# Kernel optimization log

Hardware: AMD Instinct MI355X
Metric: run time of the kernel (lower is better)

Reference implementation:

```python
import jax, jax.numpy as jnp
import numpy as np

HEADS = 4
DIM_HEAD = 32
DIM = 128
B, N, Hq, Wg = 2, 6, 32, 32   # batch, cameras, BEV grid
HK, WK = 28, 60               # image feature map


def _ln(x, g, b, eps=1e-5):
    mu = jnp.mean(x, axis=-1, keepdims=True)
    var = jnp.mean((x - mu) ** 2, axis=-1, keepdims=True)
    return (x - mu) * jax.lax.rsqrt(var + eps) * g + b


def setup_inputs() -> dict:
    key = jax.random.key(0)
    ks = jax.random.split(key, 12)
    s = 0.05  # weight scale to keep softmax logits well-conditioned
    inp = {
        'q': jax.random.normal(ks[0], (B, N, DIM, Hq, Wg), jnp.float32),
        'k': jax.random.normal(ks[1], (B, N, DIM, HK, WK), jnp.float32),
        'v': jax.random.normal(ks[2], (B, N, DIM, HK, WK), jnp.float32),
        'skip': jax.random.normal(ks[3], (B, DIM, Hq, Wg), jnp.float32),
        'q_ln_g': jnp.ones((DIM,), jnp.float32),
        'q_ln_b': jnp.zeros((DIM,), jnp.float32),
        'Wq': s * jax.random.normal(ks[4], (DIM, HEADS * DIM_HEAD), jnp.float32),
        'bq': jnp.zeros((HEADS * DIM_HEAD,), jnp.float32),
        'k_ln_g': jnp.ones((DIM,), jnp.float32),
        'k_ln_b': jnp.zeros((DIM,), jnp.float32),
        'Wk': s * jax.random.normal(ks[5], (DIM, HEADS * DIM_HEAD), jnp.float32),
        'bk': jnp.zeros((HEADS * DIM_HEAD,), jnp.float32),
        'v_ln_g': jnp.ones((DIM,), jnp.float32),
        'v_ln_b': jnp.zeros((DIM,), jnp.float32),
        'Wv': s * jax.random.normal(ks[6], (DIM, HEADS * DIM_HEAD), jnp.float32),
        'bv': jnp.zeros((HEADS * DIM_HEAD,), jnp.float32),
        'Wp': s * jax.random.normal(ks[7], (HEADS * DIM_HEAD, DIM), jnp.float32),
        'bp': jnp.zeros((DIM,), jnp.float32),
        'pre_g': jnp.ones((DIM,), jnp.float32),
        'pre_b': jnp.zeros((DIM,), jnp.float32),
        'W1': s * jax.random.normal(ks[8], (DIM, 2 * DIM), jnp.float32),
        'b1': jnp.zeros((2 * DIM,), jnp.float32),
        'W2': s * jax.random.normal(ks[9], (2 * DIM, DIM), jnp.float32),
        'b2': jnp.zeros((DIM,), jnp.float32),
        'post_g': jnp.ones((DIM,), jnp.float32),
        'post_b': jnp.zeros((DIM,), jnp.float32),
    }
    return inp


def reference(q, k, v, skip, q_ln_g, q_ln_b, Wq, bq, k_ln_g, k_ln_b, Wk, bk,
              v_ln_g, v_ln_b, Wv, bv, Wp, bp, pre_g, pre_b,
              W1, b1, W2, b2, post_g, post_b):
    b, n, d, H, W = q.shape
    Q = H * W
    K = k.shape[3] * k.shape[4]
    m, dh = HEADS, DIM_HEAD
    # b n d H W -> b n Q d   /  b n d h w -> b n K d  /  b (n K) d
    qf = q.transpose(0, 1, 3, 4, 2).reshape(b, n, Q, d)
    kf = k.transpose(0, 1, 3, 4, 2).reshape(b, n, K, d)
    vf = v.transpose(0, 1, 3, 4, 2).reshape(b, n * K, d)
    # norm -> linear, then split heads: b ... (m dh) -> (b m) ... dh
    qh = (_ln(qf, q_ln_g, q_ln_b) @ Wq + bq).reshape(b, n, Q, m, dh)
    qh = qh.transpose(0, 3, 1, 2, 4).reshape(b * m, n, Q, dh)
    kh = (_ln(kf, k_ln_g, k_ln_b) @ Wk + bk).reshape(b, n, K, m, dh)
    kh = kh.transpose(0, 3, 1, 2, 4).reshape(b * m, n, K, dh)
    vh = (_ln(vf, v_ln_g, v_ln_b) @ Wv + bv).reshape(b, n * K, m, dh)
    vh = vh.transpose(0, 2, 1, 3).reshape(b * m, n * K, dh)
    scale = dh ** -0.5
    dot = scale * jnp.einsum('anqd,ankd->anqk', qh, kh)   # (b m) n Q K
    dot = dot.transpose(0, 2, 1, 3).reshape(b * m, Q, n * K)  # fold views into keys
    att = jax.nn.softmax(dot, axis=-1)
    a = jnp.einsum('aqk,akd->aqd', att, vh)               # (b m) Q dh
    a = a.reshape(b, m, Q, dh).transpose(0, 2, 1, 3).reshape(b, Q, m * dh)
    z = a @ Wp + bp
    z = z + skip.transpose(0, 2, 3, 1).reshape(b, Q, d)
    z = _ln(z, pre_g, pre_b)
    z = z + (jax.nn.gelu(z @ W1 + b1, approximate=False) @ W2 + b2)
    z = _ln(z, post_g, post_b)
    return z.reshape(b, H, W, d).transpose(0, 3, 1, 2)
```

## Files before the change

### kernel.cpp

```cpp
#include <hip/hip_runtime.h>
#include <math.h>

#define NCAM 6
#define BSZ 2
#define SQL 1024
#define SKL 1680
#define NHEAD 4
#define DHEAD 32
#define QSCALE 0.25503494f

typedef unsigned short ushort_t;
typedef unsigned int uint_t;
typedef __attribute__((ext_vector_type(8))) short short8;
typedef __attribute__((ext_vector_type(4))) float f32x4;

#define MFMA16 __builtin_amdgcn_mfma_f32_16x16x32_bf16

__device__ __forceinline__ ushort_t f2bf(float x) {
  uint_t u = __builtin_bit_cast(uint_t, x);
  u += 0x7FFFu + ((u >> 16) & 1u);
  return (ushort_t)(u >> 16);
}

__device__ __forceinline__ float fast_gelu(float x) {
  const float ax = fabsf(x) * 0.70710678118654752f;
  const float tt = __builtin_amdgcn_rcpf(fmaf(0.3275911f, ax, 1.f));
  float poly = fmaf(tt, 1.061405429f, -1.453152027f);
  poly = fmaf(tt, poly, 1.421413741f);
  poly = fmaf(tt, poly, -0.284496736f);
  poly = fmaf(tt, poly, 0.254829592f);
  poly *= tt;
  const float e = __builtin_amdgcn_exp2f(-ax * ax * 1.4426950408889634f);
  float er = fmaf(-poly, e, 1.f);
  er = copysignf(er, x);
  return 0.5f * x * (1.f + er);
}

__global__ __launch_bounds__(256) void prep_kernel(
    const float* __restrict__ Wq, const float* __restrict__ qg, const float* __restrict__ qb, const float* __restrict__ bq,
    const float* __restrict__ Wk, const float* __restrict__ kg, const float* __restrict__ kbb, const float* __restrict__ bk,
    const float* __restrict__ Wv, const float* __restrict__ vg, const float* __restrict__ vbb, const float* __restrict__ bv,
    const float* __restrict__ Wp,
    const float* __restrict__ W1, const float* __restrict__ pre_g, const float* __restrict__ pre_b, const float* __restrict__ b1,
    const float* __restrict__ W2,
    ushort_t* WqT, ushort_t* WkT, ushort_t* WvT, ushort_t* WpT, ushort_t* W1T, ushort_t* W2T,
    float* uq, float* bbq, float* uk, float* bbk, float* uv, float* bbv, float* b1p) {
  const int mb = blockIdx.x;
  const float *W, *g = nullptr, *bln = nullptr, *bias = nullptr;
  ushort_t* WT; float *u = nullptr, *bb = nullptr;
  int kin = 128, nout = 128, ob;
  if (mb < 4)       { W=Wq; g=qg; bln=qb;   bias=bq; WT=WqT; u=uq; bb=bbq; ob=mb*32; }
  else if (mb < 8)  { W=Wk; g=kg; bln=kbb;  bias=bk; WT=WkT; u=uk; bb=bbk; ob=(mb-4)*32; }
  else if (mb < 12) { W=Wv; g=vg; bln=vbb;  bias=bv; WT=WvT; u=uv; bb=bbv; ob=(mb-8)*32; }
  else if (mb < 16) { W=Wp; WT=WpT; ob=(mb-12)*32; }
  else if (mb < 24) { W=W1; g=pre_g; bln=pre_b; bias=b1; WT=W1T; bb=b1p; nout=256; ob=(mb-16)*32; }
  else              { W=W2; WT=W2T; kin=256; ob=(mb-24)*32; }
  const int t = threadIdx.x;
  const int oc = t & 31, ig = t >> 5;
  const int out = ob + oc;
  const int nper = kin >> 3;
  float su = 0.f, sb = 0.f;
  for (int j = 0; j < nper; ++j) {
    const int in = ig * nper + j;
    const float wv_ = W[(size_t)in * nout + out];
    const float wg = g ? g[in] * wv_ : wv_;
    WT[(size_t)out * kin + in] = f2bf(wg);
    su += wg;
    if (bln) sb += bln[in] * wv_;
  }
  __shared__ float sU[8][32], sB[8][32];
  sU[ig][oc] = su; sB[ig][oc] = sb;
  __syncthreads();
  if (t < 32) {
    float tu = 0.f, tb = 0.f;
#pragma unroll
    for (int i = 0; i < 8; ++i) { tu += sU[i][t]; tb += sB[i][t]; }
    if (u)  u[ob + t] = tu;
    if (bb) bb[ob + t] = tb + (bias ? bias[ob + t] : 0.f);
  }
}

__global__ __launch_bounds__(256) void proj_mfma(
    const float* __restrict__ xq, const float* __restrict__ xk, const float* __restrict__ xv,
    const ushort_t* __restrict__ WqT, const ushort_t* __restrict__ WkT, const ushort_t* __restrict__ WvT,
    const float* __restrict__ uq, const float* __restrict__ uk, const float* __restrict__ uv,
    const float* __restrict__ bbq, const float* __restrict__ bbk, const float* __restrict__ bbv,
    ushort_t* __restrict__ Qh, ushort_t* __restrict__ Kh, ushort_t* __restrict__ Vt) {
  int blk = blockIdx.x;
  const float* x; const ushort_t* WT; const float* u; const float* bb;
  ushort_t* out; int S, ntile, vmode; float oscale;
  if (blk < 192)      { x=xq; WT=WqT; u=uq; bb=bbq; out=Qh; S=SQL; ntile=16; vmode=0; oscale=QSCALE; }
  else if (blk < 516) { blk-=192; x=xk; WT=WkT; u=uk; bb=bbk; out=Kh; S=SKL; ntile=27; vmode=0; oscale=1.f; }
  else                { blk-=516; x=xv; WT=WvT; u=uv; bb=bbv; out=Vt; S=SKL; ntile=27; vmode=1; oscale=1.f; }
  const int bn = blk / ntile;
  const int pos0 = (blk - bn * ntile) * 64;
  int valid = S - pos0; if (valid > 64) valid = 64;

  const int t = threadIdx.x;
  __shared__ ushort_t sX[64 * 128];
  __shared__ float sS1[16][64], sS2[16][64];
  __shared__ float sMu[64], sRs[64];

  {
    const int posq = t & 15, chg = t >> 4;
    int lp4 = 4 * posq; if (lp4 >= valid) lp4 = valid - 4;
    const float* xb = x + ((size_t)bn * 128 + chg * 8) * S + pos0 + lp4;
    float v[8][4];
#pragma unroll
    for (int i = 0; i < 8; ++i) {
      const float4 f = *((const float4*)(xb + (size_t)i * S));
      v[i][0] = f.x; v[i][1] = f.y; v[i][2] = f.z; v[i][3] = f.w;
    }
#pragma unroll
    for (int j = 0; j < 4; ++j) {
      float s1 = 0.f, s2 = 0.f;
#pragma unroll
      for (int i = 0; i < 8; ++i) { s1 += v[i][j]; s2 += v[i][j] * v[i][j]; }
      sS1[chg][lp4 + j] = s1; sS2[chg][lp4 + j] = s2;
    }
#pragma unroll
    for (int j = 0; j < 4; ++j) {
      const int pos = lp4 + j;
      short8 pk;
#pragma unroll
      for (int i = 0; i < 8; ++i) pk[i] = (short)f2bf(v[i][j]);
      const int phys = chg ^ (pos & 7);
      *((short8*)&sX[pos * 128 + phys * 8]) = pk;
    }
  }
  __syncthreads();
  if (t < 64) {
    float a1 = 0.f, a2 = 0.f;
#pragma unroll
    for (int g = 0; g < 16; ++g) { a1 += sS1[g][t]; a2 += sS2[g][t]; }
    const float mu = a1 * (1.f / 128.f);
    sMu[t] = mu; sRs[t] = rsqrtf(a2 * (1.f / 128.f) - mu * mu + 1e-5f);
  }
  __syncthreads();

  const int w = t >> 6, l = t & 63, lq = l & 15, quad = l >> 4;
  short8 af[2][4];
#pragma unroll
  for (int ms = 0; ms < 2; ++ms)
#pragma unroll
    for (int kk = 0; kk < 4; ++kk)
      af[ms][kk] = *((const short8*)(WT + (size_t)(w * 32 + ms * 16 + lq) * 128 + quad * 8 + kk * 32));
  f32x4 acc[4][2];
#pragma unroll
  for (int ns = 0; ns < 4; ++ns)
#pragma unroll
    for (int ms = 0; ms < 2; ++ms) acc[ns][ms] = (f32x4){0.f, 0.f, 0.f, 0.f};
#pragma unroll
  for (int ns = 0; ns < 4; ++ns) {
    short8 bf[4];
#pragma unroll
    for (int kk = 0; kk < 4; ++kk) {
      const int phys = (quad + 4 * kk) ^ (lq & 7);
      bf[kk] = *((const short8*)&sX[(ns * 16 + lq) * 128 + phys * 8]);
    }
#pragma unroll
    for (int ms = 0; ms < 2; ++ms) {
      f32x4 a = acc[ns][ms];
#pragma unroll
      for (int kk = 0; kk < 4; ++kk) a = MFMA16(af[ms][kk], bf[kk], a, 0, 0, 0);
      acc[ns][ms] = a;
    }
  }

  const int b_ = bn / NCAM, cam = bn - b_ * NCAM;
  const size_t slab = (size_t)((b_ * NHEAD + w) * NCAM + cam);
#pragma unroll
  for (int ms = 0; ms < 2; ++ms) {
    float uu[4], bv_[4];
#pragma unroll
    for (int r = 0; r < 4; ++r) {
      const int og = w * 32 + ms * 16 + quad * 4 + r;
      uu[r] = u[og]; bv_[r] = bb[og];
    }
#pragma unroll
    for (int ns = 0; ns < 4; ++ns) {
      const int p = ns * 16 + lq;
      if (p < valid) {
        const float mu = sMu[p], rs = sRs[p];
        float val[4];
#pragma unroll
        for (int r = 0; r < 4; ++r)
          val[r] = ((acc[ns][ms][r] - mu * uu[r]) * rs + bv_[r]) * oscale;
        if (vmode == 0) {
          ushort_t e0 = f2bf(val[0]), e1 = f2bf(val[1]), e2 = f2bf(val[2]), e3 = f2bf(val[3]);
          ushort_t* orow = out + (slab * S + pos0 + p) * 32 + ms * 16 + quad * 4;
          *((uint_t*)orow) = (uint_t)e0 | ((uint_t)e1 << 16);
          *((uint_t*)(orow + 2)) = (uint_t)e2 | ((uint_t)e3 << 16);
        } else {
#pragma unroll
          for (int r = 0; r < 4; ++r)
            out[(slab * 32 + ms * 16 + quad * 4 + r) * (size_t)SKL + pos0 + p] = f2bf(val[r]);
        }
      }
    }
  }
}

__global__ __launch_bounds__(512, 1) void attn_mfma(
    const ushort_t* __restrict__ Qh, const ushort_t* __restrict__ Kh,
    const ushort_t* __restrict__ Vt, ushort_t* __restrict__ Ab) {
  const int t = threadIdx.x;
  const int w = t >> 6, l = t & 63;
  const int lq = l & 15, quad = l >> 4;
  const int bm = blockIdx.x & 7;
  const int q0 = (blockIdx.x >> 3) * 32;
  const int camg = w >> 2, kq = w & 3;
  const int kstart = kq * 448;

  __shared__ ushort_t sP[8][2][2][16][72];
  __shared__ float sO[8][2][16][36];
  __shared__ float sL[8][2][16];

  f32x4 oA0 = {0.f,0.f,0.f,0.f}, oA1 = {0.f,0.f,0.f,0.f};
  f32x4 oB0 = {0.f,0.f,0.f,0.f}, oB1 = {0.f,0.f,0.f,0.f};
  float lA = 0.f, lB = 0.f;

  auto tile_full = [&](const ushort_t* Kb, const ushort_t* Vb, int kb, int buf,
                       short8 qfA, short8 qfB) {
    short8 kf[4];
#pragma unroll
    for (int st = 0; st < 4; ++st)
      kf[st] = *((const short8*)(Kb + (size_t)(kb + st * 16 + lq) * 32 + quad * 8));
    const short8 v00 = *((const short8*)(Vb + (size_t)lq * SKL + kb + quad * 8));
    const short8 v01 = *((const short8*)(Vb + (size_t)lq * SKL + kb + 32 + quad * 8));
    const short8 v10 = *((const short8*)(Vb + (size_t)(16 + lq) * SKL + kb + quad * 8));
    const short8 v11 = *((const short8*)(Vb + (size_t)(16 + lq) * SKL + kb + 32 + quad * 8));

    f32x4 sA[4], sB[4];
#pragma unroll
    for (int st = 0; st < 4; ++st) {
      f32x4 z = {0.f, 0.f, 0.f, 0.f};
      sA[st] = MFMA16(kf[st], qfA, z, 0, 0, 0);
      sB[st] = MFMA16(kf[st], qfB, z, 0, 0, 0);
    }
    float lsA = 0.f, lsB = 0.f;
#pragma unroll
    for (int st = 0; st < 4; ++st) {
      const float a0 = __builtin_amdgcn_exp2f(sA[st][0]);
      const float a1 = __builtin_amdgcn_exp2f(sA[st][1]);
      const float a2 = __builtin_amdgcn_exp2f(sA[st][2]);
      const float a3 = __builtin_amdgcn_exp2f(sA[st][3]);
      const float b0 = __builtin_amdgcn_exp2f(sB[st][0]);
      const float b1 = __builtin_amdgcn_exp2f(sB[st][1]);
      const float b2 = __builtin_amdgcn_exp2f(sB[st][2]);
      const float b3 = __builtin_amdgcn_exp2f(sB[st][3]);
      lsA += (a0 + a1) + (a2 + a3);
      lsB += (b0 + b1) + (b2 + b3);
      const uint_t pa0 = __builtin_amdgcn_perm(__builtin_bit_cast(uint_t, a1), __builtin_bit_cast(uint_t, a0), 0x07060302u);
      const uint_t pa1 = __builtin_amdgcn_perm(__builtin_bit_cast(uint_t, a3), __builtin_bit_cast(uint_t, a2), 0x07060302u);
      const uint_t pb0 = __builtin_amdgcn_perm(__builtin_bit_cast(uint_t, b1), __builtin_bit_cast(uint_t, b0), 0x07060302u);
      const uint_t pb1 = __builtin_amdgcn_perm(__builtin_bit_cast(uint_t, b3), __builtin_bit_cast(uint_t, b2), 0x07060302u);
      *((uint2*)&sP[w][buf][0][lq][st * 16 + quad * 4]) = make_uint2(pa0, pa1);
      *((uint2*)&sP[w][buf][1][lq][st * 16 + quad * 4]) = make_uint2(pb0, pb1);
    }
    const short8 pfA0 = *((const short8*)&sP[w][buf][0][lq][quad * 8]);
    const short8 pfA1 = *((const short8*)&sP[w][buf][0][lq][32 + quad * 8]);
    const short8 pfB0 = *((const short8*)&sP[w][buf][1][lq][quad * 8]);
    const short8 pfB1 = *((const short8*)&sP[w][buf][1][lq][32 + quad * 8]);
    oA0 = MFMA16(v00, pfA0, oA0, 0, 0, 0);
    oA1 = MFMA16(v10, pfA0, oA1, 0, 0, 0);
    oB0 = MFMA16(v00, pfB0, oB0, 0, 0, 0);
    oB1 = MFMA16(v10, pfB0, oB1, 0, 0, 0);
    oA0 = MFMA16(v01, pfA1, oA0, 0, 0, 0);
    oA1 = MFMA16(v11, pfA1, oA1, 0, 0, 0);
    oB0 = MFMA16(v01, pfB1, oB0, 0, 0, 0);
    oB1 = MFMA16(v11, pfB1, oB1, 0, 0, 0);
    lsA += __shfl_xor(lsA, 16, 64);
    lsA += __shfl_xor(lsA, 32, 64);
    lsB += __shfl_xor(lsB, 16, 64);
    lsB += __shfl_xor(lsB, 32, 64);
    lA += lsA; lB += lsB;
  };

  auto tile_tail = [&](const ushort_t* Kb, const ushort_t* Vb, int kb, int buf,
                       short8 qfA, short8 qfB) {
    const short8 kf = *((const short8*)(Kb + (size_t)(kb + lq) * 32 + quad * 8));
    const short8 v00 = *((const short8*)(Vb + (size_t)lq * SKL + kb + quad * 8));
    const short8 v10 = *((const short8*)(Vb + (size_t)(16 + lq) * SKL + kb + quad * 8));
    f32x4 z = {0.f, 0.f, 0.f, 0.f};
    const f32x4 s0A = MFMA16(kf, qfA, z, 0, 0, 0);
    const f32x4 s0B = MFMA16(kf, qfB, z, 0, 0, 0);
    const float a0 = __builtin_amdgcn_exp2f(s0A[0]);
    const float a1 = __builtin_amdgcn_exp2f(s0A[1]);
    const float a2 = __builtin_amdgcn_exp2f(s0A[2]);
    const float a3 = __builtin_amdgcn_exp2f(s0A[3]);
    const float b0 = __builtin_amdgcn_exp2f(s0B[0]);
    const float b1 = __builtin_amdgcn_exp2f(s0B[1]);
    const float b2 = __builtin_amdgcn_exp2f(s0B[2]);
    const float b3 = __builtin_amdgcn_exp2f(s0B[3]);
    float lsA = (a0 + a1) + (a2 + a3);
    float lsB = (b0 + b1) + (b2 + b3);
    const uint_t pa0 = __builtin_amdgcn_perm(__builtin_bit_cast(uint_t, a1), __builtin_bit_cast(uint_t, a0), 0x07060302u);
    const uint_t pa1 = __builtin_amdgcn_perm(__builtin_bit_cast(uint_t, a3), __builtin_bit_cast(uint_t, a2), 0x07060302u);
    const uint_t pb0 = __builtin_amdgcn_perm(__builtin_bit_cast(uint_t, b1), __builtin_bit_cast(uint_t, b0), 0x07060302u);
    const uint_t pb1 = __builtin_amdgcn_perm(__builtin_bit_cast(uint_t, b3), __builtin_bit_cast(uint_t, b2), 0x07060302u);
    *((uint2*)&sP[w][buf][0][lq][quad * 4]) = make_uint2(pa0, pa1);
    *((uint2*)&sP[w][buf][0][lq][16 + quad * 4]) = make_uint2(0u, 0u);
    *((uint2*)&sP[w][buf][1][lq][quad * 4]) = make_uint2(pb0, pb1);
    *((uint2*)&sP[w][buf][1][lq][16 + quad * 4]) = make_uint2(0u, 0u);
    const short8 pfA0 = *((const short8*)&sP[w][buf][0][lq][quad * 8]);
    const short8 pfB0 = *((const short8*)&sP[w][buf][1][lq][quad * 8]);
    oA0 = MFMA16(v00, pfA0, oA0, 0, 0, 0);
    oA1 = MFMA16(v10, pfA0, oA1, 0, 0, 0);
    oB0 = MFMA16(v00, pfB0, oB0, 0, 0, 0);
    oB1 = MFMA16(v10, pfB0, oB1, 0, 0, 0);
    lsA += __shfl_xor(lsA, 16, 64);
    lsA += __shfl_xor(lsA, 32, 64);
    lsB += __shfl_xor(lsB, 16, 64);
    lsB += __shfl_xor(lsB, 32, 64);
    lA += lsA; lB += lsB;
  };

  if (kq < 3) {
#pragma unroll
    for (int nc = 0; nc < 3; ++nc) {
      const int n = camg * 3 + nc;
      const ushort_t* Kb = Kh + (size_t)(bm * NCAM + n) * SKL * 32;
      const ushort_t* Vb = Vt + (size_t)(bm * NCAM + n) * 32 * SKL;
      const ushort_t* Qb = Qh + ((size_t)(bm * NCAM + n) * SQL + q0) * 32;
      const short8 qfA = *((const short8*)(Qb + (size_t)lq * 32 + quad * 8));
      const short8 qfB = *((const short8*)(Qb + (size_t)(16 + lq) * 32 + quad * 8));
#pragma unroll
      for (int kt = 0; kt < 7; ++kt)
        tile_full(Kb, Vb, kstart + kt * 64, (nc * 7 + kt) & 1, qfA, qfB);
    }
  } else {
#pragma unroll
    for (int nc = 0; nc < 3; ++nc) {
      const int n = camg * 3 + nc;
      const ushort_t* Kb = Kh + (size_t)(bm * NCAM + n) * SKL * 32;
      const ushort_t* Vb = Vt + (size_t)(bm * NCAM + n) * 32 * SKL;
      const ushort_t* Qb = Qh + ((size_t)(bm * NCAM + n) * SQL + q0) * 32;
      const short8 qfA = *((const short8*)(Qb + (size_t)lq * 32 + quad * 8));
      const short8 qfB = *((const short8*)(Qb + (size_t)(16 + lq) * 32 + quad * 8));
#pragma unroll
      for (int kt = 0; kt < 5; ++kt)
        tile_full(Kb, Vb, kstart + kt * 64, kt & 1, qfA, qfB);
      tile_tail(Kb, Vb, kstart + 320, 1, qfA, qfB);
    }
  }

  *((f32x4*)&sO[w][0][lq][quad * 4]) = oA0;
  *((f32x4*)&sO[w][0][lq][16 + quad * 4]) = oA1;
  *((f32x4*)&sO[w][1][lq][quad * 4]) = oB0;
  *((f32x4*)&sO[w][1][lq][16 + quad * 4]) = oB1;
  if (l < 16) { sL[w][0][l] = lA; sL[w][1][l] = lB; }
  __syncthreads();
  if (w < 2) {
    const int frag = w;
    float lf = 0.f;
    f32x4 a0 = {0.f, 0.f, 0.f, 0.f}, a1 = {0.f, 0.f, 0.f, 0.f};
#pragma unroll
    for (int ww = 0; ww < 8; ++ww) {
      lf += sL[ww][frag][lq];
      a0 += *((const f32x4*)&sO[ww][frag][lq][quad * 4]);
      a1 += *((const f32x4*)&sO[ww][frag][lq][16 + quad * 4]);
    }
    const float inv = 1.f / lf;
    const int b = bm >> 2, hm = bm & 3;
    ushort_t* op = Ab + ((size_t)b * SQL + q0 + frag * 16 + lq) * 128 + hm * 32 + quad * 4;
    ushort4 w0 = make_ushort4(f2bf(a0[0] * inv), f2bf(a0[1] * inv), f2bf(a0[2] * inv), f2bf(a0[3] * inv));
    ushort4 w1 = make_ushort4(f2bf(a1[0] * inv), f2bf(a1[1] * inv), f2bf(a1[2] * inv), f2bf(a1[3] * inv));
    *((ushort4*)op) = w0;
    *((ushort4*)(op + 16)) = w1;
  }
}

__global__ __launch_bounds__(256) void post_mfma(
    const ushort_t* __restrict__ Ab, const float* __restrict__ skip,
    const ushort_t* __restrict__ WpT, const float* __restrict__ bp,
    const float* __restrict__ pre_g, const float* __restrict__ pre_b,
    const ushort_t* __restrict__ W1T, const float* __restrict__ b1p,
    const ushort_t* __restrict__ W2T, const float* __restrict__ b2,
    const float* __restrict__ post_g, const float* __restrict__ post_b,
    float* __restrict__ out) {
  const int t = threadIdx.x;
  const int w = t >> 6, l = t & 63, lq = l & 15, quad = l >> 4;
  const int b = blockIdx.x >> 7;
  const int p0 = (blockIdx.x & 127) * 8;
  const int rp = (p0 + lq < SQL) ? (p0 + lq) : (SQL - 1);

  __shared__ float zf[16 * 132];
  __shared__ float sRes[16 * 132];
  __shared__ ushort_t sZb[16 * 128];
  __shared__ ushort_t sH[16 * 256];
  __shared__ float sMu[16], sRs[16];

  f32x4 z[2] = {{0.f,0.f,0.f,0.f},{0.f,0.f,0.f,0.f}};
#pragma unroll
  for (int kk = 0; kk < 4; ++kk) {
    const short8 bfr = *((const short8*)(Ab + ((size_t)b * SQL + rp) * 128 + quad * 8 + kk * 32));
#pragma unroll
    for (int ms = 0; ms < 2; ++ms) {
      const short8 afr = *((const short8*)(WpT + (size_t)(w * 32 + ms * 16 + lq) * 128 + quad * 8 + kk * 32));
      z[ms] = MFMA16(afr, bfr, z[ms], 0, 0, 0);
    }
  }
#pragma unroll
  for (int ms = 0; ms < 2; ++ms)
#pragma unroll
    for (int r = 0; r < 4; ++r) {
      const int o = w * 32 + ms * 16 + quad * 4 + r;
      const int rr = (p0 + lq < SQL) ? (p0 + lq) : (SQL - 1);
      zf[lq * 132 + o] = z[ms][r] + bp[o] + skip[(size_t)b * 131072 + (size_t)o * 1024 + rr];
    }
  __syncthreads();
  if (w == 0) {
    const int pos = l & 15, qr = l >> 4;
    float s1 = 0.f, s2 = 0.f;
#pragma unroll
    for (int j = 0; j < 32; ++j) { const float vv = zf[pos * 132 + qr * 32 + j]; s1 += vv; s2 += vv * vv; }
    s1 += __shfl_xor(s1, 16, 64); s1 += __shfl_xor(s1, 32, 64);
    s2 += __shfl_xor(s2, 16, 64); s2 += __shfl_xor(s2, 32, 64);
    const float mu = s1 * (1.f / 128.f);
    if (qr == 0) { sMu[pos] = mu; sRs[pos] = rsqrtf(s2 * (1.f / 128.f) - mu * mu + 1e-5f); }
  }
  __syncthreads();
  {
    const int pos = t & 15, grp = t >> 4;
    const float mu = sMu[pos], rs = sRs[pos];
    short8 pk;
#pragma unroll
    for (int i = 0; i < 8; ++i) {
      const int ch = grp * 8 + i;
      const float nv = (zf[pos * 132 + ch] - mu) * rs;
      pk[i] = (short)f2bf(nv);
      sRes[pos * 132 + ch] = nv * pre_g[ch] + pre_b[ch];
    }
    *((short8*)&sZb[pos * 128 + (grp ^ (pos & 7)) * 8]) = pk;
  }
  __syncthreads();
  f32x4 h[4];
#pragma unroll
  for (int ms = 0; ms < 4; ++ms) h[ms] = (f32x4){0.f, 0.f, 0.f, 0.f};
  short8 bz[4];
#pragma unroll
  for (int kk = 0; kk < 4; ++kk)
    bz[kk] = *((const short8*)&sZb[lq * 128 + ((quad + 4 * kk) ^ (lq & 7)) * 8]);
#pragma unroll
  for (int ms = 0; ms < 4; ++ms)
#pragma unroll
    for (int kk = 0; kk < 4; ++kk) {
      const short8 afr = *((const short8*)(W1T + (size_t)(w * 64 + ms * 16 + lq) * 128 + quad * 8 + kk * 32));
      h[ms] = MFMA16(afr, bz[kk], h[ms], 0, 0, 0);
    }
#pragma unroll
  for (int ms = 0; ms < 4; ++ms)
#pragma unroll
    for (int r = 0; r < 4; ++r) {
      const int o = w * 64 + ms * 16 + quad * 4 + r;
      const float hv = fast_gelu(h[ms][r] + b1p[o]);
      const int phys = (o >> 3) ^ (lq & 7);
      sH[lq * 256 + phys * 8 + (o & 7)] = f2bf(hv);
    }
  __syncthreads();
  f32x4 z2[2] = {{0.f,0.f,0.f,0.f},{0.f,0.f,0.f,0.f}};
#pragma unroll
  for (int kk = 0; kk < 8; ++kk) {
    const short8 bh = *((const short8*)&sH[lq * 256 + ((quad + 4 * kk) ^ (lq & 7)) * 8]);
#pragma unroll
    for (int ms = 0; ms < 2; ++ms) {
      const short8 afr = *((const short8*)(W2T + (size_t)(w * 32 + ms * 16 + lq) * 256 + quad * 8 + kk * 32));
      z2[ms] = MFMA16(afr, bh, z2[ms], 0, 0, 0);
    }
  }
  __syncthreads();
#pragma unroll
  for (int ms = 0; ms < 2; ++ms)
#pragma unroll
    for (int r = 0; r < 4; ++r) {
      const int o = w * 32 + ms * 16 + quad * 4 + r;
      zf[lq * 132 + o] = z2[ms][r] + b2[o] + sRes[lq * 132 + o];
    }
  __syncthreads();
  if (w == 0) {
    const int pos = l & 15, qr = l >> 4;
    float s1 = 0.f, s2 = 0.f;
#pragma unroll
    for (int j = 0; j < 32; ++j) { const float vv = zf[pos * 132 + qr * 32 + j]; s1 += vv; s2 += vv * vv; }
    s1 += __shfl_xor(s1, 16, 64); s1 += __shfl_xor(s1, 32, 64);
    s2 += __shfl_xor(s2, 16, 64); s2 += __shfl_xor(s2, 32, 64);
    const float mu = s1 * (1.f / 128.f);
    if (qr == 0) { sMu[pos] = mu; sRs[pos] = rsqrtf(s2 * (1.f / 128.f) - mu * mu + 1e-5f); }
  }
  __syncthreads();
  {
    const int pos = t & 15, grp = t >> 4;
    if (pos < 8) {
      const float mu = sMu[pos], rs = sRs[pos];
#pragma unroll
      for (int i = 0; i < 8; ++i) {
        const int ch = grp * 8 + i;
        out[(size_t)b * 131072 + (size_t)ch * 1024 + p0 + pos] =
            (zf[pos * 132 + ch] - mu) * rs * post_g[ch] + post_b[ch];
      }
    }
  }
}

extern "C" void kernel_launch(void* const* d_in, const int* in_sizes, int n_in,
                              void* d_out, int out_size, void* d_ws, size_t ws_size,
                              hipStream_t stream) {
  const float* q_in   = (const float*)d_in[0];
  const float* k_in   = (const float*)d_in[1];
  const float* v_in   = (const float*)d_in[2];
  const float* skip   = (const float*)d_in[3];
  const float* q_ln_g = (const float*)d_in[4];
  const float* q_ln_b = (const float*)d_in[5];
  const float* Wq     = (const float*)d_in[6];
  const float* bq     = (const float*)d_in[7];
  const float* k_ln_g = (const float*)d_in[8];
  const float* k_ln_b = (const float*)d_in[9];
  const float* Wk     = (const float*)d_in[10];
  const float* bk     = (const float*)d_in[11];
  const float* v_ln_g = (const float*)d_in[12];
  const float* v_ln_b = (const float*)d_in[13];
  const float* Wv     = (const float*)d_in[14];
  const float* bv     = (const float*)d_in[15];
  const float* Wp     = (const float*)d_in[16];
  const float* bp     = (const float*)d_in[17];
  const float* pre_g  = (const float*)d_in[18];
  const float* pre_b  = (const float*)d_in[19];
  const float* W1     = (const float*)d_in[20];
  const float* b1     = (const float*)d_in[21];
  const float* W2     = (const float*)d_in[22];
  const float* b2     = (const float*)d_in[23];
  const float* post_g = (const float*)d_in[24];
  const float* post_b = (const float*)d_in[25];

  char* base = (char*)d_ws;
  ushort_t* WqT = (ushort_t*)base; base += 16384 * 2;
  ushort_t* WkT = (ushort_t*)base; base += 16384 * 2;
  ushort_t* WvT = (ushort_t*)base; base += 16384 * 2;
  ushort_t* WpT = (ushort_t*)base; base += 16384 * 2;
  ushort_t* W1T = (ushort_t*)base; base += 32768 * 2;
  ushort_t* W2T = (ushort_t*)base; base += 32768 * 2;
  float* uq  = (float*)base; base += 128 * 4;
  float* bbq = (float*)base; base += 128 * 4;
  float* uk  = (float*)base; base += 128 * 4;
  float* bbk = (float*)base; base += 128 * 4;
  float* uv  = (float*)base; base += 128 * 4;
  float* bbv = (float*)base; base += 128 * 4;
  float* b1p = (float*)base; base += 256 * 4;
  base = (char*)(((size_t)base + 255) & ~(size_t)255);
  ushort_t* Qh = (ushort_t*)base; base += (size_t)1572864 * 2;
  ushort_t* Kh = (ushort_t*)base; base += (size_t)(2580480 + 4096) * 2;
  ushort_t* Vt = (ushort_t*)base; base += (size_t)(2580480 + 4096) * 2;
  ushort_t* Ab = (ushort_t*)base; base += (size_t)262144 * 2;
  float* out = (float*)d_out;

  prep_kernel<<<28, 256, 0, stream>>>(
      Wq, q_ln_g, q_ln_b, bq, Wk, k_ln_g, k_ln_b, bk, Wv, v_ln_g, v_ln_b, bv,
      Wp, W1, pre_g, pre_b, b1, W2,
      WqT, WkT, WvT, WpT, W1T, W2T, uq, bbq, uk, bbk, uv, bbv, b1p);
  proj_mfma<<<840, 256, 0, stream>>>(
      q_in, k_in, v_in, WqT, WkT, WvT, uq, uk, uv, bbq, bbk, bbv, Qh, Kh, Vt);
  attn_mfma<<<256, 512, 0, stream>>>(Qh, Kh, Vt, Ab);
  post_mfma<<<256, 256, 0, stream>>>(
      Ab, skip, WpT, bp, pre_g, pre_b, W1T, b1p, W2T, b2, post_g, post_b, out);
}
```

Before: 195.6 us.

## Split attention camera groups across blocks and raise query tile to 64

The attention kernel now assigns each block one group of three cameras for 64 queries, instead of all six cameras for 32 queries. Each wave processes flat key tiles round-robin and reuses each K/V fragment across four query fragments rather than two. Unnormalized partial outputs and row sums go to float workspace, and post_mfma combines the two camera-group partials and normalizes before the output projection. This cuts redundant K/V loads per query, at the cost of extra fp32 global traffic for the partials and more registers per wave.

```diff
diff --git a/kernel.cpp b/kernel.cpp
--- a/kernel.cpp
+++ b/kernel.cpp
@@ -203,155 +203,121 @@
 
 __global__ __launch_bounds__(512, 1) void attn_mfma(
     const ushort_t* __restrict__ Qh, const ushort_t* __restrict__ Kh,
-    const ushort_t* __restrict__ Vt, ushort_t* __restrict__ Ab) {
+    const ushort_t* __restrict__ Vt, float* __restrict__ Pa, float* __restrict__ Lp) {
   const int t = threadIdx.x;
   const int w = t >> 6, l = t & 63;
   const int lq = l & 15, quad = l >> 4;
   const int bm = blockIdx.x & 7;
-  const int q0 = (blockIdx.x >> 3) * 32;
-  const int camg = w >> 2, kq = w & 3;
-  const int kstart = kq * 448;
-
-  __shared__ ushort_t sP[8][2][2][16][72];
-  __shared__ float sO[8][2][16][36];
-  __shared__ float sL[8][2][16];
-
-  f32x4 oA0 = {0.f,0.f,0.f,0.f}, oA1 = {0.f,0.f,0.f,0.f};
-  f32x4 oB0 = {0.f,0.f,0.f,0.f}, oB1 = {0.f,0.f,0.f,0.f};
-  float lA = 0.f, lB = 0.f;
-
-  auto tile_full = [&](const ushort_t* Kb, const ushort_t* Vb, int kb, int buf,
-                       short8 qfA, short8 qfB) {
-    short8 kf[4];
-#pragma unroll
-    for (int st = 0; st < 4; ++st)
-      kf[st] = *((const short8*)(Kb + (size_t)(kb + st * 16 + lq) * 32 + quad * 8));
-    const short8 v00 = *((const short8*)(Vb + (size_t)lq * SKL + kb + quad * 8));
-    const short8 v01 = *((const short8*)(Vb + (size_t)lq * SKL + kb + 32 + quad * 8));
-    const short8 v10 = *((const short8*)(Vb + (size_t)(16 + lq) * SKL + kb + quad * 8));
-    const short8 v11 = *((const short8*)(Vb + (size_t)(16 + lq) * SKL + kb + 32 + quad * 8));
-
-    f32x4 sA[4], sB[4];
-#pragma unroll
-    for (int st = 0; st < 4; ++st) {
-      f32x4 z = {0.f, 0.f, 0.f, 0.f};
-      sA[st] = MFMA16(kf[st], qfA, z, 0, 0, 0);
-      sB[st] = MFMA16(kf[st], qfB, z, 0, 0, 0);
-    }
-    float lsA = 0.f, lsB = 0.f;
-#pragma unroll
-    for (int st = 0; st < 4; ++st) {
-      const float a0 = __builtin_amdgcn_exp2f(sA[st][0]);
-      const float a1 = __builtin_amdgcn_exp2f(sA[st][1]);
-      const float a2 = __builtin_amdgcn_exp2f(sA[st][2]);
-      const float a3 = __builtin_amdgcn_exp2f(sA[st][3]);
-      const float b0 = __builtin_amdgcn_exp2f(sB[st][0]);
-      const float b1 = __builtin_amdgcn_exp2f(sB[st][1]);
-      const float b2 = __builtin_amdgcn_exp2f(sB[st][2]);
-      const float b3 = __builtin_amdgcn_exp2f(sB[st][3]);
-      lsA += (a0 + a1) + (a2 + a3);
-      lsB += (b0 + b1) + (b2 + b3);
-      const uint_t pa0 = __builtin_amdgcn_perm(__builtin_bit_cast(uint_t, a1), __builtin_bit_cast(uint_t, a0), 0x07060302u);
-      const uint_t pa1 = __builtin_amdgcn_perm(__builtin_bit_cast(uint_t, a3), __builtin_bit_cast(uint_t, a2), 0x07060302u);
-      const uint_t pb0 = __builtin_amdgcn_perm(__builtin_bit_cast(uint_t, b1), __builtin_bit_cast(uint_t, b0), 0x07060302u);
-      const uint_t pb1 = __builtin_amdgcn_perm(__builtin_bit_cast(uint_t, b3), __builtin_bit_cast(uint_t, b2), 0x07060302u);
-      *((uint2*)&sP[w][buf][0][lq][st * 16 + quad * 4]) = make_uint2(pa0, pa1);
-      *((uint2*)&sP[w][buf][1][lq][st * 16 + quad * 4]) = make_uint2(pb0, pb1);
-    }
-    const short8 pfA0 = *((const short8*)&sP[w][buf][0][lq][quad * 8]);
-    const short8 pfA1 = *((const short8*)&sP[w][buf][0][lq][32 + quad * 8]);
-    const short8 pfB0 = *((const short8*)&sP[w][buf][1][lq][quad * 8]);
-    const short8 pfB1 = *((const short8*)&sP[w][buf][1][lq][32 + quad * 8]);
-    oA0 = MFMA16(v00, pfA0, oA0, 0, 0, 0);
-    oA1 = MFMA16(v10, pfA0, oA1, 0, 0, 0);
-    oB0 = MFMA16(v00, pfB0, oB0, 0, 0, 0);
-    oB1 = MFMA16(v10, pfB0, oB1, 0, 0, 0);
-    oA0 = MFMA16(v01, pfA1, oA0, 0, 0, 0);
-    oA1 = MFMA16(v11, pfA1, oA1, 0, 0, 0);
-    oB0 = MFMA16(v01, pfB1, oB0, 0, 0, 0);
-    oB1 = MFMA16(v11, pfB1, oB1, 0, 0, 0);
-    lsA += __shfl_xor(lsA, 16, 64);
-    lsA += __shfl_xor(lsA, 32, 64);
-    lsB += __shfl_xor(lsB, 16, 64);
-    lsB += __shfl_xor(lsB, 32, 64);
-    lA += lsA; lB += lsB;
-  };
-
-  auto tile_tail = [&](const ushort_t* Kb, const ushort_t* Vb, int kb, int buf,
-                       short8 qfA, short8 qfB) {
-    const short8 kf = *((const short8*)(Kb + (size_t)(kb + lq) * 32 + quad * 8));
-    const short8 v00 = *((const short8*)(Vb + (size_t)lq * SKL + kb + quad * 8));
-    const short8 v10 = *((const short8*)(Vb + (size_t)(16 + lq) * SKL + kb + quad * 8));
-    f32x4 z = {0.f, 0.f, 0.f, 0.f};
-    const f32x4 s0A = MFMA16(kf, qfA, z, 0, 0, 0);
-    const f32x4 s0B = MFMA16(kf, qfB, z, 0, 0, 0);
-    const float a0 = __builtin_amdgcn_exp2f(s0A[0]);
-    const float a1 = __builtin_amdgcn_exp2f(s0A[1]);
-    const float a2 = __builtin_amdgcn_exp2f(s0A[2]);
-    const float a3 = __builtin_amdgcn_exp2f(s0A[3]);
-    const float b0 = __builtin_amdgcn_exp2f(s0B[0]);
-    const float b1 = __builtin_amdgcn_exp2f(s0B[1]);
-    const float b2 = __builtin_amdgcn_exp2f(s0B[2]);
-    const float b3 = __builtin_amdgcn_exp2f(s0B[3]);
-    float lsA = (a0 + a1) + (a2 + a3);
-    float lsB = (b0 + b1) + (b2 + b3);
-    const uint_t pa0 = __builtin_amdgcn_perm(__builtin_bit_cast(uint_t, a1), __builtin_bit_cast(uint_t, a0), 0x07060302u);
-    const uint_t pa1 = __builtin_amdgcn_perm(__builtin_bit_cast(uint_t, a3), __builtin_bit_cast(uint_t, a2), 0x07060302u);
-    const uint_t pb0 = __builtin_amdgcn_perm(__builtin_bit_cast(uint_t, b1), __builtin_bit_cast(uint_t, b0), 0x07060302u);
-    const uint_t pb1 = __builtin_amdgcn_perm(__builtin_bit_cast(uint_t, b3), __builtin_bit_cast(uint_t, b2), 0x07060302u);
-    *((uint2*)&sP[w][buf][0][lq][quad * 4]) = make_uint2(pa0, pa1);
-    *((uint2*)&sP[w][buf][0][lq][16 + quad * 4]) = make_uint2(0u, 0u);
-    *((uint2*)&sP[w][buf][1][lq][quad * 4]) = make_uint2(pb0, pb1);
-    *((uint2*)&sP[w][buf][1][lq][16 + quad * 4]) = make_uint2(0u, 0u);
-    const short8 pfA0 = *((const short8*)&sP[w][buf][0][lq][quad * 8]);
-    const short8 pfB0 = *((const short8*)&sP[w][buf][1][lq][quad * 8]);
-    oA0 = MFMA16(v00, pfA0, oA0, 0, 0, 0);
-    oA1 = MFMA16(v10, pfA0, oA1, 0, 0, 0);
-    oB0 = MFMA16(v00, pfB0, oB0, 0, 0, 0);
-    oB1 = MFMA16(v10, pfB0, oB1, 0, 0, 0);
-    lsA += __shfl_xor(lsA, 16, 64);
-    lsA += __shfl_xor(lsA, 32, 64);
-    lsB += __shfl_xor(lsB, 16, 64);
-    lsB += __shfl_xor(lsB, 32, 64);
-    lA += lsA; lB += lsB;
-  };
-
-  if (kq < 3) {
-#pragma unroll
-    for (int nc = 0; nc < 3; ++nc) {
-      const int n = camg * 3 + nc;
-      const ushort_t* Kb = Kh + (size_t)(bm * NCAM + n) * SKL * 32;
-      const ushort_t* Vb = Vt + (size_t)(bm * NCAM + n) * 32 * SKL;
+  const int c = (blockIdx.x >> 3) & 1;
+  const int q0 = (blockIdx.x >> 4) * 64;
+
+  __shared__ __align__(16) unsigned char smem[75776];
+  ushort_t (*sP)[4][16][72] = (ushort_t(*)[4][16][72])smem;
+  float (*sO)[4][16][36] = (float(*)[4][16][36])smem;
+  float (*sL)[4][16] = (float(*)[4][16])(smem + 73728);
+
+  f32x4 o[4][2];
+#pragma unroll
+  for (int f = 0; f < 4; ++f) { o[f][0] = (f32x4){0.f,0.f,0.f,0.f}; o[f][1] = (f32x4){0.f,0.f,0.f,0.f}; }
+  float lsum[4] = {0.f, 0.f, 0.f, 0.f};
+
+  int cur_cam = -1;
+  const ushort_t* Kb = nullptr;
+  const ushort_t* Vb = nullptr;
+  short8 qf[4];
+
+  for (int s = w; s < 81; s += 8) {
+    const int cl = (s >= 54) ? 2 : ((s >= 27) ? 1 : 0);
+    const int tile = s - cl * 27;
+    if (cl != cur_cam) {
+      cur_cam = cl;
+      const int n = c * 3 + cl;
+      Kb = Kh + (size_t)(bm * NCAM + n) * SKL * 32;
+      Vb = Vt + (size_t)(bm * NCAM + n) * 32 * SKL;
       const ushort_t* Qb = Qh + ((size_t)(bm * NCAM + n) * SQL + q0) * 32;
-      const short8 qfA = *((const short8*)(Qb + (size_t)lq * 32 + quad * 8));
-      const short8 qfB = *((const short8*)(Qb + (size_t)(16 + lq) * 32 + quad * 8));
-#pragma unroll
-      for (int kt = 0; kt < 7; ++kt)
-        tile_full(Kb, Vb, kstart + kt * 64, (nc * 7 + kt) & 1, qfA, qfB);
-    }
-  } else {
-#pragma unroll
-    for (int nc = 0; nc < 3; ++nc) {
-      const int n = camg * 3 + nc;
-      const ushort_t* Kb = Kh + (size_t)(bm * NCAM + n) * SKL * 32;
-      const ushort_t* Vb = Vt + (size_t)(bm * NCAM + n) * 32 * SKL;
-      const ushort_t* Qb = Qh + ((size_t)(bm * NCAM + n) * SQL + q0) * 32;
-      const short8 qfA = *((const short8*)(Qb + (size_t)lq * 32 + quad * 8));
-      const short8 qfB = *((const short8*)(Qb + (size_t)(16 + lq) * 32 + quad * 8));
-#pragma unroll
-      for (int kt = 0; kt < 5; ++kt)
-        tile_full(Kb, Vb, kstart + kt * 64, kt & 1, qfA, qfB);
-      tile_tail(Kb, Vb, kstart + 320, 1, qfA, qfB);
-    }
-  }
-
-  *((f32x4*)&sO[w][0][lq][quad * 4]) = oA0;
-  *((f32x4*)&sO[w][0][lq][16 + quad * 4]) = oA1;
-  *((f32x4*)&sO[w][1][lq][quad * 4]) = oB0;
-  *((f32x4*)&sO[w][1][lq][16 + quad * 4]) = oB1;
-  if (l < 16) { sL[w][0][l] = lA; sL[w][1][l] = lB; }
-  __syncthreads();
-  if (w < 2) {
+#pragma unroll
+      for (int f = 0; f < 4; ++f)
+        qf[f] = *((const short8*)(Qb + (size_t)(f * 16 + lq) * 32 + quad * 8));
+    }
+    if (tile < 26) {
+      const int kb = tile * 64;
+      short8 kf[4];
+#pragma unroll
+      for (int st = 0; st < 4; ++st)
+        kf[st] = *((const short8*)(Kb + (size_t)(kb + st * 16 + lq) * 32 + quad * 8));
+      const short8 v00 = *((const short8*)(Vb + (size_t)lq * SKL + kb + quad * 8));
+      const short8 v01 = *((const short8*)(Vb + (size_t)lq * SKL + kb + 32 + quad * 8));
+      const short8 v10 = *((const short8*)(Vb + (size_t)(16 + lq) * SKL + kb + quad * 8));
+      const short8 v11 = *((const short8*)(Vb + (size_t)(16 + lq) * SKL + kb + 32 + quad * 8));
+#pragma unroll
+      for (int f = 0; f < 4; ++f) {
+        f32x4 sfr[4];
+#pragma unroll
+        for (int st = 0; st < 4; ++st) {
+          f32x4 z = {0.f, 0.f, 0.f, 0.f};
+          sfr[st] = MFMA16(kf[st], qf[f], z, 0, 0, 0);
+        }
+        float ls = 0.f;
+#pragma unroll
+        for (int st = 0; st < 4; ++st) {
+          const float e0 = __builtin_amdgcn_exp2f(sfr[st][0]);
+          const float e1 = __builtin_amdgcn_exp2f(sfr[st][1]);
+          const float e2 = __builtin_amdgcn_exp2f(sfr[st][2]);
+          const float e3 = __builtin_amdgcn_exp2f(sfr[st][3]);
+          ls += (e0 + e1) + (e2 + e3);
+          const uint_t pa = __builtin_amdgcn_perm(__builtin_bit_cast(uint_t, e1), __builtin_bit_cast(uint_t, e0), 0x07060302u);
+          const uint_t pb = __builtin_amdgcn_perm(__builtin_bit_cast(uint_t, e3), __builtin_bit_cast(uint_t, e2), 0x07060302u);
+          *((uint2*)&sP[w][f][lq][st * 16 + quad * 4]) = make_uint2(pa, pb);
+        }
+        const short8 pf0 = *((const short8*)&sP[w][f][lq][quad * 8]);
+        const short8 pf1 = *((const short8*)&sP[w][f][lq][32 + quad * 8]);
+        o[f][0] = MFMA16(v00, pf0, o[f][0], 0, 0, 0);
+        o[f][1] = MFMA16(v10, pf0, o[f][1], 0, 0, 0);
+        o[f][0] = MFMA16(v01, pf1, o[f][0], 0, 0, 0);
+        o[f][1] = MFMA16(v11, pf1, o[f][1], 0, 0, 0);
+        ls += __shfl_xor(ls, 16, 64);
+        ls += __shfl_xor(ls, 32, 64);
+        lsum[f] += ls;
+      }
+    } else {
+      const int kb = 1664;
+      const short8 kf0 = *((const short8*)(Kb + (size_t)(kb + lq) * 32 + quad * 8));
+      const short8 v00 = *((const short8*)(Vb + (size_t)lq * SKL + kb + quad * 8));
+      const short8 v10 = *((const short8*)(Vb + (size_t)(16 + lq) * SKL + kb + quad * 8));
+#pragma unroll
+      for (int f = 0; f < 4; ++f) {
+        f32x4 z = {0.f, 0.f, 0.f, 0.f};
+        const f32x4 s0 = MFMA16(kf0, qf[f], z, 0, 0, 0);
+        const float e0 = __builtin_amdgcn_exp2f(s0[0]);
+        const float e1 = __builtin_amdgcn_exp2f(s0[1]);
+        const float e2 = __builtin_amdgcn_exp2f(s0[2]);
+        const float e3 = __builtin_amdgcn_exp2f(s0[3]);
+        float ls = (e0 + e1) + (e2 + e3);
+        const uint_t pa = __builtin_amdgcn_perm(__builtin_bit_cast(uint_t, e1), __builtin_bit_cast(uint_t, e0), 0x07060302u);
+        const uint_t pb = __builtin_amdgcn_perm(__builtin_bit_cast(uint_t, e3), __builtin_bit_cast(uint_t, e2), 0x07060302u);
+        *((uint2*)&sP[w][f][lq][quad * 4]) = make_uint2(pa, pb);
+        *((uint2*)&sP[w][f][lq][16 + quad * 4]) = make_uint2(0u, 0u);
+        const short8 pf0 = *((const short8*)&sP[w][f][lq][quad * 8]);
+        o[f][0] = MFMA16(v00, pf0, o[f][0], 0, 0, 0);
+        o[f][1] = MFMA16(v10, pf0, o[f][1], 0, 0, 0);
+        ls += __shfl_xor(ls, 16, 64);
+        ls += __shfl_xor(ls, 32, 64);
+        lsum[f] += ls;
+      }
+    }
+  }
+
+#pragma unroll
+  for (int f = 0; f < 4; ++f) {
+    *((f32x4*)&sO[w][f][lq][quad * 4]) = o[f][0];
+    *((f32x4*)&sO[w][f][lq][16 + quad * 4]) = o[f][1];
+  }
+  if (l < 16) {
+#pragma unroll
+    for (int f = 0; f < 4; ++f) sL[w][f][l] = lsum[f];
+  }
+  __syncthreads();
+  if (w < 4) {
     const int frag = w;
     float lf = 0.f;
     f32x4 a0 = {0.f, 0.f, 0.f, 0.f}, a1 = {0.f, 0.f, 0.f, 0.f};
@@ -361,18 +327,17 @@
       a0 += *((const f32x4*)&sO[ww][frag][lq][quad * 4]);
       a1 += *((const f32x4*)&sO[ww][frag][lq][16 + quad * 4]);
     }
-    const float inv = 1.f / lf;
-    const int b = bm >> 2, hm = bm & 3;
-    ushort_t* op = Ab + ((size_t)b * SQL + q0 + frag * 16 + lq) * 128 + hm * 32 + quad * 4;
-    ushort4 w0 = make_ushort4(f2bf(a0[0] * inv), f2bf(a0[1] * inv), f2bf(a0[2] * inv), f2bf(a0[3] * inv));
-    ushort4 w1 = make_ushort4(f2bf(a1[0] * inv), f2bf(a1[1] * inv), f2bf(a1[2] * inv), f2bf(a1[3] * inv));
-    *((ushort4*)op) = w0;
-    *((ushort4*)(op + 16)) = w1;
+    const int row = q0 + frag * 16 + lq;
+    const size_t base = (((size_t)(c * 8 + bm)) * SQL + row) * 32;
+    *((f32x4*)(Pa + base + quad * 4)) = a0;
+    *((f32x4*)(Pa + base + 16 + quad * 4)) = a1;
+    if (l < 16) Lp[((size_t)(c * 8 + bm)) * SQL + row] = lf;
   }
 }
 
 __global__ __launch_bounds__(256) void post_mfma(
-    const ushort_t* __restrict__ Ab, const float* __restrict__ skip,
+    const float* __restrict__ Pa, const float* __restrict__ Lp,
+    const float* __restrict__ skip,
     const ushort_t* __restrict__ WpT, const float* __restrict__ bp,
     const float* __restrict__ pre_g, const float* __restrict__ pre_b,
     const ushort_t* __restrict__ W1T, const float* __restrict__ b1p,
@@ -394,7 +359,20 @@
   f32x4 z[2] = {{0.f,0.f,0.f,0.f},{0.f,0.f,0.f,0.f}};
 #pragma unroll
   for (int kk = 0; kk < 4; ++kk) {
-    const short8 bfr = *((const short8*)(Ab + ((size_t)b * SQL + rp) * 128 + quad * 8 + kk * 32));
+    const size_t i0 = (((size_t)(b * 4 + kk)) * SQL + rp) * 32 + quad * 8;
+    const size_t i1 = (((size_t)(8 + b * 4 + kk)) * SQL + rp) * 32 + quad * 8;
+    const f32x4 p0a = *((const f32x4*)(Pa + i0));
+    const f32x4 p0b = *((const f32x4*)(Pa + i0 + 4));
+    const f32x4 p1a = *((const f32x4*)(Pa + i1));
+    const f32x4 p1b = *((const f32x4*)(Pa + i1 + 4));
+    const float inv = 1.f / (Lp[((size_t)(b * 4 + kk)) * SQL + rp] +
+                             Lp[((size_t)(8 + b * 4 + kk)) * SQL + rp]);
+    short8 bfr;
+#pragma unroll
+    for (int j = 0; j < 4; ++j) {
+      bfr[j] = (short)f2bf((p0a[j] + p1a[j]) * inv);
+      bfr[4 + j] = (short)f2bf((p0b[j] + p1b[j]) * inv);
+    }
 #pragma unroll
     for (int ms = 0; ms < 2; ++ms) {
       const short8 afr = *((const short8*)(WpT + (size_t)(w * 32 + ms * 16 + lq) * 128 + quad * 8 + kk * 32));
@@ -406,8 +384,7 @@
 #pragma unroll
     for (int r = 0; r < 4; ++r) {
       const int o = w * 32 + ms * 16 + quad * 4 + r;
-      const int rr = (p0 + lq < SQL) ? (p0 + lq) : (SQL - 1);
-      zf[lq * 132 + o] = z[ms][r] + bp[o] + skip[(size_t)b * 131072 + (size_t)o * 1024 + rr];
+      zf[lq * 132 + o] = z[ms][r] + bp[o] + skip[(size_t)b * 131072 + (size_t)o * 1024 + rp];
     }
   __syncthreads();
   if (w == 0) {
@@ -551,7 +528,9 @@
   ushort_t* Qh = (ushort_t*)base; base += (size_t)1572864 * 2;
   ushort_t* Kh = (ushort_t*)base; base += (size_t)(2580480 + 4096) * 2;
   ushort_t* Vt = (ushort_t*)base; base += (size_t)(2580480 + 4096) * 2;
-  ushort_t* Ab = (ushort_t*)base; base += (size_t)262144 * 2;
+  base = (char*)(((size_t)base + 255) & ~(size_t)255);
+  float* Pa = (float*)base; base += (size_t)2 * 8 * SQL * 32 * 4;
+  float* Lp = (float*)base; base += (size_t)2 * 8 * SQL * 4;
   float* out = (float*)d_out;
 
   prep_kernel<<<28, 256, 0, stream>>>(
@@ -560,7 +539,7 @@
       WqT, WkT, WvT, WpT, W1T, W2T, uq, bbq, uk, bbk, uv, bbv, b1p);
   proj_mfma<<<840, 256, 0, stream>>>(
       q_in, k_in, v_in, WqT, WkT, WvT, uq, uk, uv, bbq, bbk, bbv, Qh, Kh, Vt);
-  attn_mfma<<<256, 512, 0, stream>>>(Qh, Kh, Vt, Ab);
+  attn_mfma<<<256, 512, 0, stream>>>(Qh, Kh, Vt, Pa, Lp);
   post_mfma<<<256, 256, 0, stream>>>(
-      Ab, skip, WpT, bp, pre_g, pre_b, W1T, b1p, W2T, b2, post_g, post_b, out);
-}
+      Pa, Lp, skip, WpT, bp, pre_g, pre_b, W1T, b1p, W2T, b2, post_g, post_b, out);
+}
```

Result: faster. 172.5 us (-11.8%).
